# Kernel tuning notes

Hardware: AMD Instinct MI355X
Metric: run time of the kernel (lower is better)

## Reference

```python
import jax, jax.numpy as jnp
import numpy as np

N_NODES = 10000
N_EDGES = 60000
D = 128          # latent_size
L = 15           # num_layers
EPS = 1e-5       # LayerNorm eps (torch default)


def _layernorm(h, g, b):
    mu = jnp.mean(h, axis=-1, keepdims=True)
    var = jnp.mean(jnp.square(h - mu), axis=-1, keepdims=True)
    return (h - mu) * jax.lax.rsqrt(var + EPS) * g + b


def _mlp(h, w1, b1, g1, bt1, w2, b2, g2, bt2):
    # Linear -> LayerNorm -> GELU(exact) -> [Dropout: identity in eval] -> Linear -> LayerNorm
    h = _layernorm(h @ w1 + b1, g1, bt1)
    h = jax.nn.gelu(h, approximate=False)
    return _layernorm(h @ w2 + b2, g2, bt2)


def setup_inputs() -> dict:
    key = jax.random.key(0)
    ks = jax.random.split(key, 20)
    x = jax.random.normal(ks[0], (N_NODES, D), dtype=jnp.float32)
    edge_index = jax.random.randint(ks[1], (2, N_EDGES), 0, N_NODES, dtype=jnp.int32)
    edge_attr = jax.random.normal(ks[2], (N_EDGES, D), dtype=jnp.float32)
    s = 0.02
    # Edge MLP params: Linear(3D->2D), LN(2D), Linear(2D->D), LN(D), stacked over L layers
    ew1 = jax.random.normal(ks[3], (L, 3 * D, 2 * D), dtype=jnp.float32) * s
    eb1 = jnp.zeros((L, 2 * D), dtype=jnp.float32)
    eg1 = jnp.ones((L, 2 * D), dtype=jnp.float32)
    ebt1 = jnp.zeros((L, 2 * D), dtype=jnp.float32)
    ew2 = jax.random.normal(ks[4], (L, 2 * D, D), dtype=jnp.float32) * s
    eb2 = jnp.zeros((L, D), dtype=jnp.float32)
    eg2 = jnp.ones((L, D), dtype=jnp.float32)
    ebt2 = jnp.zeros((L, D), dtype=jnp.float32)
    # Node MLP params: Linear(2D->2D), LN(2D), Linear(2D->D), LN(D)
    nw1 = jax.random.normal(ks[5], (L, 2 * D, 2 * D), dtype=jnp.float32) * s
    nb1 = jnp.zeros((L, 2 * D), dtype=jnp.float32)
    ng1 = jnp.ones((L, 2 * D), dtype=jnp.float32)
    nbt1 = jnp.zeros((L, 2 * D), dtype=jnp.float32)
    nw2 = jax.random.normal(ks[6], (L, 2 * D, D), dtype=jnp.float32) * s
    nb2 = jnp.zeros((L, D), dtype=jnp.float32)
    ng2 = jnp.ones((L, D), dtype=jnp.float32)
    nbt2 = jnp.zeros((L, D), dtype=jnp.float32)
    return dict(x=x, edge_index=edge_index, edge_attr=edge_attr,
                ew1=ew1, eb1=eb1, eg1=eg1, ebt1=ebt1, ew2=ew2, eb2=eb2, eg2=eg2, ebt2=ebt2,
                nw1=nw1, nb1=nb1, ng1=ng1, nbt1=nbt1, nw2=nw2, nb2=nb2, ng2=ng2, nbt2=nbt2)


def reference(x, edge_index, edge_attr,
              ew1, eb1, eg1, ebt1, ew2, eb2, eg2, ebt2,
              nw1, nb1, ng1, nbt1, nw2, nb2, ng2, nbt2):
    row, col = edge_index[0], edge_index[1]
    # neighbor counts (per destination node), clamped to >= 1; constant across layers
    count = jax.ops.segment_sum(jnp.ones((edge_index.shape[1],), dtype=x.dtype), col,
                                num_segments=x.shape[0])
    count = jnp.maximum(count, 1.0)[:, None]  # [N,1]
    for i in range(L):
        edge_input = jnp.concatenate([x[row], x[col], edge_attr], axis=1)  # [E, 3D]
        edge_attr = edge_attr + _mlp(edge_input, ew1[i], eb1[i], eg1[i], ebt1[i],
                                     ew2[i], eb2[i], eg2[i], ebt2[i])
        agg = jax.ops.segment_sum(edge_attr, col, num_segments=x.shape[0]) / count  # [N, D]
        node_input = jnp.concatenate([x, agg], axis=1)  # [N, 2D]
        x = x + _mlp(node_input, nw1[i], nb1[i], ng1[i], nbt1[i],
                     nw2[i], nb2[i], ng2[i], nbt2[i])
    return x, edge_attr
```

## Files before the change

### kernel.cpp

```cpp
#include <hip/hip_runtime.h>
#include <hip/hip_bf16.h>
#include <math.h>

#define NN 10000
#define NE 60000
#define DD 128
#define NL 15
#define LN_EPS 1e-5f

typedef __attribute__((ext_vector_type(8))) short short8;
typedef __attribute__((ext_vector_type(4))) float floatx4;

__device__ __forceinline__ unsigned short f2bf(float f) {
    unsigned u = __float_as_uint(f);
    u += 0x7fff + ((u >> 16) & 1);
    return (unsigned short)(u >> 16);
}
__device__ __forceinline__ unsigned bc2(float a, float b) {
    __hip_bfloat162 t = __float22bfloat162_rn(make_float2(a, b));
    return *(unsigned*)&t;
}
__device__ __forceinline__ float gelu_fast(float y) {
    float u = y * y;
    float s2 = y * fmaf(u, 0.07135481283f, 1.59576912161f);
    return y * __builtin_amdgcn_rcpf(1.0f + __expf(-s2));
}

__device__ __forceinline__ void pack_one(const float* __restrict__ W, unsigned short* __restrict__ P,
                                         int u, int Kk, int Nk, bool perm) {
    int per_layer = Kk * Nk;
    int i = u / per_layer;
    int v0 = u - i * per_layer;
    int S = Kk >> 5;
    int t = v0 / (S * 512);
    int rem = v0 - t * (S * 512);
    int s = rem >> 9;
    int v = rem & 511;
    int l = v >> 3, j = v & 7;
    int kv = (s << 5) + ((l >> 4) << 3) + j;
    int k = perm ? (((kv & 15) << 4) | (kv >> 4)) : kv;
    int n = (t << 4) + (l & 15);
    P[u] = f2bf(W[((size_t)i * Kk + k) * Nk + n]);
}

#define N_EW1 (NL * 384 * 256)
#define N_EW2 (NL * 256 * 128)
#define N_NW1 (NL * 256 * 256)
#define N_NW2 (NL * 256 * 128)

__global__ void pack_all(const float* __restrict__ ew1, const float* __restrict__ ew2,
                         const float* __restrict__ nw1, const float* __restrict__ nw2,
                         unsigned short* __restrict__ P) {
    int tid = blockIdx.x * blockDim.x + threadIdx.x;
    if (tid < N_EW1) { pack_one(ew1, P, tid, 384, 256, false); return; }
    tid -= N_EW1;
    if (tid < N_EW2) { pack_one(ew2, P + N_EW1, tid, 256, 128, true); return; }
    tid -= N_EW2;
    if (tid < N_NW1) { pack_one(nw1, P + N_EW1 + N_EW2, tid, 256, 256, false); return; }
    tid -= N_NW1;
    if (tid < N_NW2) { pack_one(nw2, P + N_EW1 + N_EW2 + N_NW1, tid, 256, 128, true); return; }
}

__global__ void hist_kernel(const int* __restrict__ ecol, int* __restrict__ cnt) {
    int e = blockIdx.x * blockDim.x + threadIdx.x;
    if (e < NE) atomicAdd(&cnt[ecol[e]], 1);
}

__global__ void scan_kernel(const int* __restrict__ cnt, int* __restrict__ starts,
                            int* __restrict__ cursor, float* __restrict__ cinv) {
    __shared__ int part[256];
    int t = threadIdx.x;
    const int chunk = (NN + 255) / 256;
    int lo = t * chunk;
    int hi = lo + chunk; if (hi > NN) hi = NN;
    int s = 0;
    for (int n = lo; n < hi; ++n) s += cnt[n];
    part[t] = s;
    __syncthreads();
    for (int off = 1; off < 256; off <<= 1) {
        int v = (t >= off) ? part[t - off] : 0;
        __syncthreads();
        part[t] += v;
        __syncthreads();
    }
    int base = part[t] - s;
    for (int n = lo; n < hi; ++n) {
        int c = cnt[n];
        starts[n] = base; cursor[n] = base;
        cinv[n] = 1.0f / (float)(c > 0 ? c : 1);
        base += c;
    }
}

__global__ void fill_kernel(const int* __restrict__ ecol, int* __restrict__ cursor,
                            int* __restrict__ eidx) {
    int e = blockIdx.x * blockDim.x + threadIdx.x;
    if (e < NE) {
        int slot = atomicAdd(&cursor[ecol[e]], 1);
        eidx[slot] = e;
    }
}

__global__ __launch_bounds__(256)
void agg_kernel(const float* __restrict__ ea, const int* __restrict__ starts,
                const int* __restrict__ cnt, const float* __restrict__ cinv,
                const int* __restrict__ eidx, float* __restrict__ agg) {
    int n = blockIdx.x * 4 + (threadIdx.x >> 6);
    if (n >= NN) return;
    int lane = threadIdx.x & 63;
    int st = starts[n], de = cnt[n];
    float sx = 0.f, sy = 0.f;
    for (int i = 0; i < de; ++i) {
        int e = eidx[st + i];
        const float2 v = *(const float2*)&ea[(size_t)e * DD + lane * 2];
        sx += v.x; sy += v.y;
    }
    float ci = cinv[n];
    float2 o; o.x = sx * ci; o.y = sy * ci;
    *(float2*)&agg[(size_t)n * DD + lane * 2] = o;
}

template <int K1, int ROWS_TOTAL, bool EDGE>
__global__ __launch_bounds__(256, 4)
void mlp_mfma(const float* __restrict__ xin,
              const int* __restrict__ erow, const int* __restrict__ ecol,
              const float* __restrict__ aux,
              float* __restrict__ target,
              const unsigned short* __restrict__ W1p, const unsigned short* __restrict__ W2p,
              const float* __restrict__ b1, const float* __restrict__ g1, const float* __restrict__ bt1,
              const float* __restrict__ b2, const float* __restrict__ g2, const float* __restrict__ bt2)
{
    constexpr int S1 = K1 / 32;
    constexpr int ROWS = 32;
    constexpr int NIT = K1 / 64;
    __shared__ union {
        unsigned short a1[ROWS * K1];
        unsigned short h[ROWS * 256];
    } sm;
    __shared__ float red1[ROWS][8];
    __shared__ float red2[ROWS][4];

    const int tid  = threadIdx.x;
    const int lane = tid & 63;
    const int w    = tid >> 6;
    const int q    = lane >> 4;
    const int c15  = lane & 15;
    const int r0   = blockIdx.x * ROWS;

    {
        const int r = tid >> 3;
        const int g = tid & 7;
        const int row_g = r0 + r;
        const bool ok = (ROWS_TOTAL % ROWS == 0) || (row_g < ROWS_TOTAL);
        const float* baseA;
        const float* baseB;
        const float* baseC = nullptr;
        if (EDGE) {
            baseA = &xin[(size_t)erow[row_g] * DD];
            baseB = &xin[(size_t)ecol[row_g] * DD];
            baseC = &target[(size_t)row_g * DD];
        } else {
            baseA = ok ? &xin[(size_t)row_g * DD] : nullptr;
            baseB = ok ? &aux[(size_t)row_g * DD] : nullptr;
        }
        #pragma unroll
        for (int it = 0; it < NIT; ++it) {
            const int p = (g + 8 * it) << 3;
            float4 v0 = make_float4(0.f, 0.f, 0.f, 0.f);
            float4 v1 = v0;
            if (!EDGE ? ok : true) {
                const float* src;
                if (p < 128)      src = baseA + p;
                else if (p < 256) src = baseB + (p - 128);
                else              src = baseC + (p - 256);
                v0 = *(const float4*)src;
                v1 = *(const float4*)(src + 4);
            }
            int addr = r * K1 + ((((g + 8 * it) ^ (r & 7)) << 3));
            uint4 pk;
            pk.x = bc2(v0.x, v0.y); pk.y = bc2(v0.z, v0.w);
            pk.z = bc2(v1.x, v1.y); pk.w = bc2(v1.z, v1.w);
            *(uint4*)&sm.a1[addr] = pk;
        }
    }
    __syncthreads();

    floatx4 acc[2][4];
    #pragma unroll
    for (int mt = 0; mt < 2; ++mt)
        #pragma unroll
        for (int ntl = 0; ntl < 4; ++ntl)
            acc[mt][ntl] = (floatx4){0.f, 0.f, 0.f, 0.f};

    #pragma unroll
    for (int s = 0; s < S1; ++s) {
        short8 af[2];
        #pragma unroll
        for (int mt = 0; mt < 2; ++mt) {
            int row  = (mt << 4) + c15;
            int kgrp = ((s << 2) + q) ^ (row & 7);
            af[mt] = *(const short8*)&sm.a1[row * K1 + (kgrp << 3)];
        }
        #pragma unroll
        for (int ntl = 0; ntl < 4; ++ntl) {
            const short8 bf = *(const short8*)&W1p[((((((w << 2) + ntl) * S1) + s) << 6) + lane) << 3];
            #pragma unroll
            for (int mt = 0; mt < 2; ++mt)
                acc[mt][ntl] = __builtin_amdgcn_mfma_f32_16x16x32_bf16(af[mt], bf, acc[mt][ntl], 0, 0, 0);
        }
    }

    float b1c[4], g1c[4], t1c[4];
    #pragma unroll
    for (int ntl = 0; ntl < 4; ++ntl) {
        int col = (((w << 2) + ntl) << 4) + c15;
        b1c[ntl] = b1[col]; g1c[ntl] = g1[col]; t1c[ntl] = bt1[col];
    }
    #pragma unroll
    for (int mt = 0; mt < 2; ++mt)
        #pragma unroll
        for (int r = 0; r < 4; ++r) {
            float p = 0.f, sq = 0.f;
            #pragma unroll
            for (int ntl = 0; ntl < 4; ++ntl) {
                float v = acc[mt][ntl][r] + b1c[ntl];
                acc[mt][ntl][r] = v;
                p += v; sq += v * v;
            }
            p += __shfl_xor(p, 1);  sq += __shfl_xor(sq, 1);
            p += __shfl_xor(p, 2);  sq += __shfl_xor(sq, 2);
            p += __shfl_xor(p, 4);  sq += __shfl_xor(sq, 4);
            p += __shfl_xor(p, 8);  sq += __shfl_xor(sq, 8);
            if (c15 == 0) {
                int row = (mt << 4) + (q << 2) + r;
                red1[row][(w << 1) + 0] = p;
                red1[row][(w << 1) + 1] = sq;
            }
        }
    __syncthreads();

    #pragma unroll
    for (int mt = 0; mt < 2; ++mt)
        #pragma unroll
        for (int r = 0; r < 4; ++r) {
            int row = (mt << 4) + (q << 2) + r;
            const float4 p0 = *(const float4*)&red1[row][0];
            const float4 p1 = *(const float4*)&red1[row][4];
            float p  = p0.x + p0.z + p1.x + p1.z;
            float sq = p0.y + p0.w + p1.y + p1.w;
            float mu = p * (1.0f / 256.0f);
            float rs = rsqrtf(sq * (1.0f / 256.0f) - mu * mu + LN_EPS);
            float y0 = gelu_fast((acc[mt][0][r] - mu) * rs * g1c[0] + t1c[0]);
            float y1 = gelu_fast((acc[mt][1][r] - mu) * rs * g1c[1] + t1c[1]);
            float y2 = gelu_fast((acc[mt][2][r] - mu) * rs * g1c[2] + t1c[2]);
            float y3 = gelu_fast((acc[mt][3][r] - mu) * rs * g1c[3] + t1c[3]);
            uint2 hp;
            hp.x = bc2(y0, y1);
            hp.y = bc2(y2, y3);
            int gg = (c15 << 1) + (w >> 1);
            int addr = row * 256 + (((gg ^ (row & 7)) << 3) | ((w & 1) << 2));
            *(uint2*)&sm.h[addr] = hp;
        }
    __syncthreads();

    floatx4 acc2[4];
    #pragma unroll
    for (int j = 0; j < 4; ++j) acc2[j] = (floatx4){0.f, 0.f, 0.f, 0.f};

    const int mrow = ((w & 1) << 4) + c15;
    const int nh   = w >> 1;
    #pragma unroll
    for (int s = 0; s < 8; ++s) {
        int kgrp = ((s << 2) + q) ^ (mrow & 7);
        const short8 a = *(const short8*)&sm.h[mrow * 256 + (kgrp << 3)];
        #pragma unroll
        for (int j = 0; j < 4; ++j) {
            int nt = (nh << 2) + j;
            const short8 b = *(const short8*)&W2p[((((nt << 3) + s) << 6) + lane) << 3];
            acc2[j] = __builtin_amdgcn_mfma_f32_16x16x32_bf16(a, b, acc2[j], 0, 0, 0);
        }
    }

    float b2c[4], g2c[4], t2c[4];
    #pragma unroll
    for (int j = 0; j < 4; ++j) {
        int col = (((nh << 2) + j) << 4) + c15;
        b2c[j] = b2[col]; g2c[j] = g2[col]; t2c[j] = bt2[col];
    }
    #pragma unroll
    for (int r = 0; r < 4; ++r) {
        float p = 0.f, sq = 0.f;
        #pragma unroll
        for (int j = 0; j < 4; ++j) {
            float v = acc2[j][r] + b2c[j];
            acc2[j][r] = v;
            p += v; sq += v * v;
        }
        p += __shfl_xor(p, 1);  sq += __shfl_xor(sq, 1);
        p += __shfl_xor(p, 2);  sq += __shfl_xor(sq, 2);
        p += __shfl_xor(p, 4);  sq += __shfl_xor(sq, 4);
        p += __shfl_xor(p, 8);  sq += __shfl_xor(sq, 8);
        if (c15 == 0) {
            int row = ((w & 1) << 4) + (q << 2) + r;
            red2[row][(nh << 1) + 0] = p;
            red2[row][(nh << 1) + 1] = sq;
        }
    }
    __syncthreads();

    #pragma unroll
    for (int r = 0; r < 4; ++r) {
        int row = ((w & 1) << 4) + (q << 2) + r;
        const float4 pp = *(const float4*)&red2[row][0];
        float p  = pp.x + pp.z;
        float sq = pp.y + pp.w;
        float mu = p * (1.0f / 128.0f);
        float rs = rsqrtf(sq * (1.0f / 128.0f) - mu * mu + LN_EPS);
        int rowg = r0 + row;
        if (ROWS_TOTAL % ROWS == 0 || rowg < ROWS_TOTAL) {
            #pragma unroll
            for (int j = 0; j < 4; ++j) {
                int col = (((nh << 2) + j) << 4) + c15;
                float o = (acc2[j][r] - mu) * rs * g2c[j] + t2c[j];
                target[(size_t)rowg * DD + col] += o;
            }
        }
    }
}

extern "C" void kernel_launch(void* const* d_in, const int* in_sizes, int n_in,
                              void* d_out, int out_size, void* d_ws, size_t ws_size,
                              hipStream_t stream) {
    const float* x_in  = (const float*)d_in[0];
    const int*   ei    = (const int*)  d_in[1];
    const float* ea_in = (const float*)d_in[2];
    const float* ew1 = (const float*)d_in[3];
    const float* eb1 = (const float*)d_in[4];
    const float* eg1 = (const float*)d_in[5];
    const float* ebt1= (const float*)d_in[6];
    const float* ew2 = (const float*)d_in[7];
    const float* eb2 = (const float*)d_in[8];
    const float* eg2 = (const float*)d_in[9];
    const float* ebt2= (const float*)d_in[10];
    const float* nw1 = (const float*)d_in[11];
    const float* nb1 = (const float*)d_in[12];
    const float* ng1 = (const float*)d_in[13];
    const float* nbt1= (const float*)d_in[14];
    const float* nw2 = (const float*)d_in[15];
    const float* nb2 = (const float*)d_in[16];
    const float* ng2 = (const float*)d_in[17];
    const float* nbt2= (const float*)d_in[18];

    const int* erow = ei;
    const int* ecol = ei + NE;

    float* xbuf  = (float*)d_out;
    float* eabuf = (float*)d_out + NN * DD;

    unsigned short* ew1p = (unsigned short*)d_ws;
    unsigned short* ew2p = ew1p + N_EW1;
    unsigned short* nw1p = ew2p + N_EW2;
    unsigned short* nw2p = nw1p + N_NW1;
    int*   cnt    = (int*)(nw2p + N_NW2);
    int*   starts = cnt + NN;
    int*   cursor = starts + NN;
    int*   eidx   = cursor + NN;
    float* cinv   = (float*)(eidx + NE);
    float* agg    = cinv + NN;

    hipMemcpyAsync(xbuf,  x_in,  (size_t)NN * DD * sizeof(float), hipMemcpyDeviceToDevice, stream);
    hipMemcpyAsync(eabuf, ea_in, (size_t)NE * DD * sizeof(float), hipMemcpyDeviceToDevice, stream);

    hipMemsetAsync(cnt, 0, NN * sizeof(int), stream);
    hist_kernel<<<(NE + 255) / 256, 256, 0, stream>>>(ecol, cnt);
    scan_kernel<<<1, 256, 0, stream>>>(cnt, starts, cursor, cinv);
    fill_kernel<<<(NE + 255) / 256, 256, 0, stream>>>(ecol, cursor, eidx);

    {
        int ntot = N_EW1 + N_EW2 + N_NW1 + N_NW2;
        pack_all<<<(ntot + 255) / 256, 256, 0, stream>>>(ew1, ew2, nw1, nw2, ew1p);
    }

    for (int i = 0; i < NL; ++i) {
        mlp_mfma<384, NE, true><<<NE / 32, 256, 0, stream>>>(
            xbuf, erow, ecol, nullptr, eabuf,
            ew1p + (size_t)i * 384 * 256, ew2p + (size_t)i * 256 * 128,
            eb1 + (size_t)i * 256, eg1 + (size_t)i * 256, ebt1 + (size_t)i * 256,
            eb2 + (size_t)i * 128, eg2 + (size_t)i * 128, ebt2 + (size_t)i * 128);
        agg_kernel<<<(NN + 3) / 4, 256, 0, stream>>>(eabuf, starts, cnt, cinv, eidx, agg);
        mlp_mfma<256, NN, false><<<(NN + 31) / 32, 256, 0, stream>>>(
            xbuf, nullptr, nullptr, agg, xbuf,
            nw1p + (size_t)i * 256 * 256, nw2p + (size_t)i * 256 * 128,
            nb1 + (size_t)i * 256, ng1 + (size_t)i * 256, nbt1 + (size_t)i * 256,
            nb2 + (size_t)i * 128, ng2 + (size_t)i * 128, nbt2 + (size_t)i * 128);
    }
}
```

Measured before the change: 1.291 ms.

## Double MLP row tile to 64 and give each wave full output rows

Each block now handles 64 rows instead of 32, so every weight fragment loaded from global memory feeds four M-tiles in the first GEMM rather than two. The second GEMM is remapped so each wave owns 16 full rows across all 128 output columns. This lets the final LayerNorm reduce entirely within the wave and drops the red2 shared buffer and one barrier. In exchange the kernel uses more registers and shared memory (the 384-wide edge tile is 48KB), which can lower occupancy under launch_bounds(256,4), and the last partial node tile is handled by clamping the row index.

Result: slower. 1.712 ms (+32.5%).

```diff
diff --git a/kernel.cpp b/kernel.cpp
--- a/kernel.cpp
+++ b/kernel.cpp
@@ -131,14 +131,13 @@
               const float* __restrict__ b2, const float* __restrict__ g2, const float* __restrict__ bt2)
 {
     constexpr int S1 = K1 / 32;
-    constexpr int ROWS = 32;
-    constexpr int NIT = K1 / 64;
+    constexpr int ROWS = 64;
+    constexpr int NIT = K1 / 32;
     __shared__ union {
         unsigned short a1[ROWS * K1];
         unsigned short h[ROWS * 256];
     } sm;
     __shared__ float red1[ROWS][8];
-    __shared__ float red2[ROWS][4];
 
     const int tid  = threadIdx.x;
     const int lane = tid & 63;
@@ -148,35 +147,33 @@
     const int r0   = blockIdx.x * ROWS;
 
     {
-        const int r = tid >> 3;
-        const int g = tid & 7;
+        const int r = tid >> 2;
+        const int g = tid & 3;
         const int row_g = r0 + r;
         const bool ok = (ROWS_TOTAL % ROWS == 0) || (row_g < ROWS_TOTAL);
+        const int rg = ok ? row_g : 0;
         const float* baseA;
         const float* baseB;
         const float* baseC = nullptr;
         if (EDGE) {
-            baseA = &xin[(size_t)erow[row_g] * DD];
-            baseB = &xin[(size_t)ecol[row_g] * DD];
-            baseC = &target[(size_t)row_g * DD];
+            baseA = &xin[(size_t)erow[rg] * DD];
+            baseB = &xin[(size_t)ecol[rg] * DD];
+            baseC = &target[(size_t)rg * DD];
         } else {
-            baseA = ok ? &xin[(size_t)row_g * DD] : nullptr;
-            baseB = ok ? &aux[(size_t)row_g * DD] : nullptr;
+            baseA = &xin[(size_t)rg * DD];
+            baseB = &aux[(size_t)rg * DD];
         }
         #pragma unroll
         for (int it = 0; it < NIT; ++it) {
-            const int p = (g + 8 * it) << 3;
-            float4 v0 = make_float4(0.f, 0.f, 0.f, 0.f);
-            float4 v1 = v0;
-            if (!EDGE ? ok : true) {
-                const float* src;
-                if (p < 128)      src = baseA + p;
-                else if (p < 256) src = baseB + (p - 128);
-                else              src = baseC + (p - 256);
-                v0 = *(const float4*)src;
-                v1 = *(const float4*)(src + 4);
-            }
-            int addr = r * K1 + ((((g + 8 * it) ^ (r & 7)) << 3));
+            const int pg = g + (it << 2);
+            const int p  = pg << 3;
+            const float* src;
+            if (p < 128)      src = baseA + p;
+            else if (p < 256) src = baseB + (p - 128);
+            else              src = baseC + (p - 256);
+            float4 v0 = *(const float4*)src;
+            float4 v1 = *(const float4*)(src + 4);
+            int addr = r * K1 + ((pg ^ (r & 7)) << 3);
             uint4 pk;
             pk.x = bc2(v0.x, v0.y); pk.y = bc2(v0.z, v0.w);
             pk.z = bc2(v1.x, v1.y); pk.w = bc2(v1.z, v1.w);
@@ -185,18 +182,18 @@
     }
     __syncthreads();
 
-    floatx4 acc[2][4];
-    #pragma unroll
-    for (int mt = 0; mt < 2; ++mt)
+    floatx4 acc[4][4];
+    #pragma unroll
+    for (int mt = 0; mt < 4; ++mt)
         #pragma unroll
         for (int ntl = 0; ntl < 4; ++ntl)
             acc[mt][ntl] = (floatx4){0.f, 0.f, 0.f, 0.f};
 
     #pragma unroll
     for (int s = 0; s < S1; ++s) {
-        short8 af[2];
-        #pragma unroll
-        for (int mt = 0; mt < 2; ++mt) {
+        short8 af[4];
+        #pragma unroll
+        for (int mt = 0; mt < 4; ++mt) {
             int row  = (mt << 4) + c15;
             int kgrp = ((s << 2) + q) ^ (row & 7);
             af[mt] = *(const short8*)&sm.a1[row * K1 + (kgrp << 3)];
@@ -205,7 +202,7 @@
         for (int ntl = 0; ntl < 4; ++ntl) {
             const short8 bf = *(const short8*)&W1p[((((((w << 2) + ntl) * S1) + s) << 6) + lane) << 3];
             #pragma unroll
-            for (int mt = 0; mt < 2; ++mt)
+            for (int mt = 0; mt < 4; ++mt)
                 acc[mt][ntl] = __builtin_amdgcn_mfma_f32_16x16x32_bf16(af[mt], bf, acc[mt][ntl], 0, 0, 0);
         }
     }
@@ -217,7 +214,7 @@
         b1c[ntl] = b1[col]; g1c[ntl] = g1[col]; t1c[ntl] = bt1[col];
     }
     #pragma unroll
-    for (int mt = 0; mt < 2; ++mt)
+    for (int mt = 0; mt < 4; ++mt)
         #pragma unroll
         for (int r = 0; r < 4; ++r) {
             float p = 0.f, sq = 0.f;
@@ -240,7 +237,7 @@
     __syncthreads();
 
     #pragma unroll
-    for (int mt = 0; mt < 2; ++mt)
+    for (int mt = 0; mt < 4; ++mt)
         #pragma unroll
         for (int r = 0; r < 4; ++r) {
             int row = (mt << 4) + (q << 2) + r;
@@ -263,35 +260,33 @@
         }
     __syncthreads();
 
-    floatx4 acc2[4];
-    #pragma unroll
-    for (int j = 0; j < 4; ++j) acc2[j] = (floatx4){0.f, 0.f, 0.f, 0.f};
-
-    const int mrow = ((w & 1) << 4) + c15;
-    const int nh   = w >> 1;
+    floatx4 acc2[8];
+    #pragma unroll
+    for (int j = 0; j < 8; ++j) acc2[j] = (floatx4){0.f, 0.f, 0.f, 0.f};
+
+    const int mrow = (w << 4) + c15;
     #pragma unroll
     for (int s = 0; s < 8; ++s) {
         int kgrp = ((s << 2) + q) ^ (mrow & 7);
         const short8 a = *(const short8*)&sm.h[mrow * 256 + (kgrp << 3)];
         #pragma unroll
-        for (int j = 0; j < 4; ++j) {
-            int nt = (nh << 2) + j;
-            const short8 b = *(const short8*)&W2p[((((nt << 3) + s) << 6) + lane) << 3];
+        for (int j = 0; j < 8; ++j) {
+            const short8 b = *(const short8*)&W2p[((((j << 3) + s) << 6) + lane) << 3];
             acc2[j] = __builtin_amdgcn_mfma_f32_16x16x32_bf16(a, b, acc2[j], 0, 0, 0);
         }
     }
 
-    float b2c[4], g2c[4], t2c[4];
-    #pragma unroll
-    for (int j = 0; j < 4; ++j) {
-        int col = (((nh << 2) + j) << 4) + c15;
+    float b2c[8], g2c[8], t2c[8];
+    #pragma unroll
+    for (int j = 0; j < 8; ++j) {
+        int col = (j << 4) + c15;
         b2c[j] = b2[col]; g2c[j] = g2[col]; t2c[j] = bt2[col];
     }
     #pragma unroll
     for (int r = 0; r < 4; ++r) {
         float p = 0.f, sq = 0.f;
         #pragma unroll
-        for (int j = 0; j < 4; ++j) {
+        for (int j = 0; j < 8; ++j) {
             float v = acc2[j][r] + b2c[j];
             acc2[j][r] = v;
             p += v; sq += v * v;
@@ -300,27 +295,14 @@
         p += __shfl_xor(p, 2);  sq += __shfl_xor(sq, 2);
         p += __shfl_xor(p, 4);  sq += __shfl_xor(sq, 4);
         p += __shfl_xor(p, 8);  sq += __shfl_xor(sq, 8);
-        if (c15 == 0) {
-            int row = ((w & 1) << 4) + (q << 2) + r;
-            red2[row][(nh << 1) + 0] = p;
-            red2[row][(nh << 1) + 1] = sq;
-        }
-    }
-    __syncthreads();
-
-    #pragma unroll
-    for (int r = 0; r < 4; ++r) {
-        int row = ((w & 1) << 4) + (q << 2) + r;
-        const float4 pp = *(const float4*)&red2[row][0];
-        float p  = pp.x + pp.z;
-        float sq = pp.y + pp.w;
         float mu = p * (1.0f / 128.0f);
         float rs = rsqrtf(sq * (1.0f / 128.0f) - mu * mu + LN_EPS);
+        int row  = (w << 4) + (q << 2) + r;
         int rowg = r0 + row;
         if (ROWS_TOTAL % ROWS == 0 || rowg < ROWS_TOTAL) {
             #pragma unroll
-            for (int j = 0; j < 4; ++j) {
-                int col = (((nh << 2) + j) << 4) + c15;
+            for (int j = 0; j < 8; ++j) {
+                int col = (j << 4) + c15;
                 float o = (acc2[j][r] - mu) * rs * g2c[j] + t2c[j];
                 target[(size_t)rowg * DD + col] += o;
             }
@@ -382,13 +364,13 @@
     }
 
     for (int i = 0; i < NL; ++i) {
-        mlp_mfma<384, NE, true><<<NE / 32, 256, 0, stream>>>(
+        mlp_mfma<384, NE, true><<<(NE + 63) / 64, 256, 0, stream>>>(
             xbuf, erow, ecol, nullptr, eabuf,
             ew1p + (size_t)i * 384 * 256, ew2p + (size_t)i * 256 * 128,
             eb1 + (size_t)i * 256, eg1 + (size_t)i * 256, ebt1 + (size_t)i * 256,
             eb2 + (size_t)i * 128, eg2 + (size_t)i * 128, ebt2 + (size_t)i * 128);
         agg_kernel<<<(NN + 3) / 4, 256, 0, stream>>>(eabuf, starts, cnt, cinv, eidx, agg);
-        mlp_mfma<256, NN, false><<<(NN + 31) / 32, 256, 0, stream>>>(
+        mlp_mfma<256, NN, false><<<(NN + 63) / 64, 256, 0, stream>>>(
             xbuf, nullptr, nullptr, agg, xbuf,
             nw1p + (size_t)i * 256 * 256, nw2p + (size_t)i * 256 * 128,
             nb1 + (size_t)i * 256, ng1 + (size_t)i * 256, nbt1 + (size_t)i * 256,
```

## Keep bf16 shadow copies of node and edge features and load MFMA operands directly

Applied to the files above, without the earlier changes.

Adds bf16 shadow buffers for x, edge_attr and the aggregate. The MLP epilogue updates both the fp32 master and its bf16 shadow. The MLP kernel now loads A-operand fragments straight from the bf16 shadows in global memory, dropping the fp32 gather, the conversion into LDS and a barrier. The aggregation kernel reads and writes bf16, which halves its gather traffic. Launch bounds are raised to allow more resident blocks. The trade-offs are extra shadow writes, less coalesced per-lane fragment loads from global memory, and bf16 rounding inside the aggregation sum.

Result: slower. 1.704 ms (+32.0%).

```diff
diff --git a/kernel.cpp b/kernel.cpp
--- a/kernel.cpp
+++ b/kernel.cpp
@@ -59,6 +59,23 @@
     if (tid < N_NW1) { pack_one(nw1, P + N_EW1 + N_EW2, tid, 256, 256, false); return; }
     tid -= N_NW1;
     if (tid < N_NW2) { pack_one(nw2, P + N_EW1 + N_EW2 + N_NW1, tid, 256, 128, true); return; }
+}
+
+__global__ void cvt_shadow(const float* __restrict__ xf, const float* __restrict__ eaf,
+                           unsigned short* __restrict__ xb, unsigned short* __restrict__ eab) {
+    int i = blockIdx.x * blockDim.x + threadIdx.x;
+    const int NX = NN * DD / 4;
+    const int NEA = NE * DD / 4;
+    if (i < NX) {
+        float4 v = ((const float4*)xf)[i];
+        uint2 p; p.x = bc2(v.x, v.y); p.y = bc2(v.z, v.w);
+        ((uint2*)xb)[i] = p;
+    } else if (i < NX + NEA) {
+        int j = i - NX;
+        float4 v = ((const float4*)eaf)[j];
+        uint2 p; p.x = bc2(v.x, v.y); p.y = bc2(v.z, v.w);
+        ((uint2*)eab)[j] = p;
+    }
 }
 
 __global__ void hist_kernel(const int* __restrict__ ecol, int* __restrict__ cnt) {
@@ -102,9 +119,9 @@
 }
 
 __global__ __launch_bounds__(256)
-void agg_kernel(const float* __restrict__ ea, const int* __restrict__ starts,
+void agg_kernel(const unsigned short* __restrict__ eab, const int* __restrict__ starts,
                 const int* __restrict__ cnt, const float* __restrict__ cinv,
-                const int* __restrict__ eidx, float* __restrict__ agg) {
+                const int* __restrict__ eidx, unsigned short* __restrict__ aggb) {
     int n = blockIdx.x * 4 + (threadIdx.x >> 6);
     if (n >= NN) return;
     int lane = threadIdx.x & 63;
@@ -112,31 +129,28 @@
     float sx = 0.f, sy = 0.f;
     for (int i = 0; i < de; ++i) {
         int e = eidx[st + i];
-        const float2 v = *(const float2*)&ea[(size_t)e * DD + lane * 2];
-        sx += v.x; sy += v.y;
+        unsigned u = *(const unsigned*)&eab[(size_t)e * DD + lane * 2];
+        sx += __uint_as_float(u << 16);
+        sy += __uint_as_float(u & 0xffff0000u);
     }
     float ci = cinv[n];
-    float2 o; o.x = sx * ci; o.y = sy * ci;
-    *(float2*)&agg[(size_t)n * DD + lane * 2] = o;
+    *(unsigned*)&aggb[(size_t)n * DD + lane * 2] = bc2(sx * ci, sy * ci);
 }
 
 template <int K1, int ROWS_TOTAL, bool EDGE>
-__global__ __launch_bounds__(256, 4)
-void mlp_mfma(const float* __restrict__ xin,
+__global__ __launch_bounds__(256, 6)
+void mlp_mfma(const unsigned short* __restrict__ xbf,
               const int* __restrict__ erow, const int* __restrict__ ecol,
-              const float* __restrict__ aux,
+              const unsigned short* __restrict__ auxbf,
               float* __restrict__ target,
+              unsigned short* __restrict__ shadow,
               const unsigned short* __restrict__ W1p, const unsigned short* __restrict__ W2p,
               const float* __restrict__ b1, const float* __restrict__ g1, const float* __restrict__ bt1,
               const float* __restrict__ b2, const float* __restrict__ g2, const float* __restrict__ bt2)
 {
     constexpr int S1 = K1 / 32;
     constexpr int ROWS = 32;
-    constexpr int NIT = K1 / 64;
-    __shared__ union {
-        unsigned short a1[ROWS * K1];
-        unsigned short h[ROWS * 256];
-    } sm;
+    __shared__ unsigned short hsm[ROWS * 256];
     __shared__ float red1[ROWS][8];
     __shared__ float red2[ROWS][4];
 
@@ -147,43 +161,22 @@
     const int c15  = lane & 15;
     const int r0   = blockIdx.x * ROWS;
 
-    {
-        const int r = tid >> 3;
-        const int g = tid & 7;
-        const int row_g = r0 + r;
-        const bool ok = (ROWS_TOTAL % ROWS == 0) || (row_g < ROWS_TOTAL);
-        const float* baseA;
-        const float* baseB;
-        const float* baseC = nullptr;
+    const unsigned short* aB0[2];
+    const unsigned short* aB1[2];
+    const unsigned short* aB2[2];
+    #pragma unroll
+    for (int mt = 0; mt < 2; ++mt) {
+        int rm = r0 + (mt << 4) + c15;
+        if (ROWS_TOTAL % ROWS != 0 && rm >= ROWS_TOTAL) rm = 0;
         if (EDGE) {
-            baseA = &xin[(size_t)erow[row_g] * DD];
-            baseB = &xin[(size_t)ecol[row_g] * DD];
-            baseC = &target[(size_t)row_g * DD];
+            aB0[mt] = xbf + (size_t)erow[rm] * DD;
+            aB1[mt] = xbf + (size_t)ecol[rm] * DD;
+            aB2[mt] = auxbf + (size_t)rm * DD;
         } else {
-            baseA = ok ? &xin[(size_t)row_g * DD] : nullptr;
-            baseB = ok ? &aux[(size_t)row_g * DD] : nullptr;
-        }
-        #pragma unroll
-        for (int it = 0; it < NIT; ++it) {
-            const int p = (g + 8 * it) << 3;
-            float4 v0 = make_float4(0.f, 0.f, 0.f, 0.f);
-            float4 v1 = v0;
-            if (!EDGE ? ok : true) {
-                const float* src;
-                if (p < 128)      src = baseA + p;
-                else if (p < 256) src = baseB + (p - 128);
-                else              src = baseC + (p - 256);
-                v0 = *(const float4*)src;
-                v1 = *(const float4*)(src + 4);
-            }
-            int addr = r * K1 + ((((g + 8 * it) ^ (r & 7)) << 3));
-            uint4 pk;
-            pk.x = bc2(v0.x, v0.y); pk.y = bc2(v0.z, v0.w);
-            pk.z = bc2(v1.x, v1.y); pk.w = bc2(v1.z, v1.w);
-            *(uint4*)&sm.a1[addr] = pk;
-        }
-    }
-    __syncthreads();
+            aB0[mt] = xbf + (size_t)rm * DD;
+            aB1[mt] = auxbf + (size_t)rm * DD;
+        }
+    }
 
     floatx4 acc[2][4];
     #pragma unroll
@@ -194,12 +187,15 @@
 
     #pragma unroll
     for (int s = 0; s < S1; ++s) {
+        const int koff = (s << 5) + (q << 3);
         short8 af[2];
         #pragma unroll
         for (int mt = 0; mt < 2; ++mt) {
-            int row  = (mt << 4) + c15;
-            int kgrp = ((s << 2) + q) ^ (row & 7);
-            af[mt] = *(const short8*)&sm.a1[row * K1 + (kgrp << 3)];
+            const unsigned short* src;
+            if (s < 4)      src = aB0[mt] + koff;
+            else if (s < 8) src = aB1[mt] + (koff - 128);
+            else            src = aB2[mt] + (koff - 256);
+            af[mt] = *(const short8*)src;
         }
         #pragma unroll
         for (int ntl = 0; ntl < 4; ++ntl) {
@@ -259,7 +255,7 @@
             hp.y = bc2(y2, y3);
             int gg = (c15 << 1) + (w >> 1);
             int addr = row * 256 + (((gg ^ (row & 7)) << 3) | ((w & 1) << 2));
-            *(uint2*)&sm.h[addr] = hp;
+            *(uint2*)&hsm[addr] = hp;
         }
     __syncthreads();
 
@@ -272,7 +268,7 @@
     #pragma unroll
     for (int s = 0; s < 8; ++s) {
         int kgrp = ((s << 2) + q) ^ (mrow & 7);
-        const short8 a = *(const short8*)&sm.h[mrow * 256 + (kgrp << 3)];
+        const short8 a = *(const short8*)&hsm[mrow * 256 + (kgrp << 3)];
         #pragma unroll
         for (int j = 0; j < 4; ++j) {
             int nt = (nh << 2) + j;
@@ -322,7 +318,10 @@
             for (int j = 0; j < 4; ++j) {
                 int col = (((nh << 2) + j) << 4) + c15;
                 float o = (acc2[j][r] - mu) * rs * g2c[j] + t2c[j];
-                target[(size_t)rowg * DD + col] += o;
+                size_t off = (size_t)rowg * DD + col;
+                float nv = target[off] + o;
+                target[off] = nv;
+                shadow[off] = f2bf(nv);
             }
         }
     }
@@ -361,15 +360,22 @@
     unsigned short* ew2p = ew1p + N_EW1;
     unsigned short* nw1p = ew2p + N_EW2;
     unsigned short* nw2p = nw1p + N_NW1;
-    int*   cnt    = (int*)(nw2p + N_NW2);
+    unsigned short* x_bf  = nw2p + N_NW2;
+    unsigned short* ea_bf = x_bf + NN * DD;
+    unsigned short* agg_bf= ea_bf + NE * DD;
+    int*   cnt    = (int*)(agg_bf + NN * DD);
     int*   starts = cnt + NN;
     int*   cursor = starts + NN;
     int*   eidx   = cursor + NN;
     float* cinv   = (float*)(eidx + NE);
-    float* agg    = cinv + NN;
 
     hipMemcpyAsync(xbuf,  x_in,  (size_t)NN * DD * sizeof(float), hipMemcpyDeviceToDevice, stream);
     hipMemcpyAsync(eabuf, ea_in, (size_t)NE * DD * sizeof(float), hipMemcpyDeviceToDevice, stream);
+
+    {
+        int ntot = (NN * DD + NE * DD) / 4;
+        cvt_shadow<<<(ntot + 255) / 256, 256, 0, stream>>>(x_in, ea_in, x_bf, ea_bf);
+    }
 
     hipMemsetAsync(cnt, 0, NN * sizeof(int), stream);
     hist_kernel<<<(NE + 255) / 256, 256, 0, stream>>>(ecol, cnt);
@@ -383,13 +389,13 @@
 
     for (int i = 0; i < NL; ++i) {
         mlp_mfma<384, NE, true><<<NE / 32, 256, 0, stream>>>(
-            xbuf, erow, ecol, nullptr, eabuf,
+            x_bf, erow, ecol, ea_bf, eabuf, ea_bf,
             ew1p + (size_t)i * 384 * 256, ew2p + (size_t)i * 256 * 128,
             eb1 + (size_t)i * 256, eg1 + (size_t)i * 256, ebt1 + (size_t)i * 256,
             eb2 + (size_t)i * 128, eg2 + (size_t)i * 128, ebt2 + (size_t)i * 128);
-        agg_kernel<<<(NN + 3) / 4, 256, 0, stream>>>(eabuf, starts, cnt, cinv, eidx, agg);
+        agg_kernel<<<(NN + 3) / 4, 256, 0, stream>>>(ea_bf, starts, cnt, cinv, eidx, agg_bf);
         mlp_mfma<256, NN, false><<<(NN + 31) / 32, 256, 0, stream>>>(
-            xbuf, nullptr, nullptr, agg, xbuf,
+            x_bf, nullptr, nullptr, agg_bf, xbuf, x_bf,
             nw1p + (size_t)i * 256 * 256, nw2p + (size_t)i * 256 * 128,
             nb1 + (size_t)i * 256, ng1 + (size_t)i * 256, nbt1 + (size_t)i * 256,
             nb2 + (size_t)i * 128, ng2 + (size_t)i * 128, nbt2 + (size_t)i * 128);
```
